# Kernel optimization log

Measured on AMD Instinct MI355X. Metric: run time of the kernel, lower is better.

Reference implementation:

```python
import jax, jax.numpy as jnp
import numpy as np

N, E, MUL, ATTR, NBASIS = 30000, 480000, 32, 8, 8
AVG_NEIGH = 16.0
INV_SQRT3 = 1.0 / np.sqrt(3.0).astype(np.float32)  # wigner 3j (1,1,0)
LOG2 = float(np.log(2.0))


def ssp(x):
    # shifted softplus: softplus(x) - log(2)
    return jax.nn.softplus(x) - LOG2


def setup_inputs() -> dict:
    key = jax.random.key(0)
    ks = jax.random.split(key, 15)
    return {
        "node_s": jax.random.normal(ks[0], (N, MUL), jnp.float32),
        "node_v": jax.random.normal(ks[1], (N, MUL, 3), jnp.float32),
        "node_attr": jax.random.uniform(ks[2], (N, ATTR), jnp.float32),
        "edge_attr": jax.random.normal(ks[3], (E, 4), jnp.float32),       # [sh0 | sh1(3)]
        "edge_scalars": jax.random.uniform(ks[4], (E, NBASIS), jnp.float32),
        "W1_0": jax.random.normal(ks[5], (MUL, MUL), jnp.float32),
        "W1_1": jax.random.normal(ks[6], (MUL, MUL), jnp.float32),
        "Wfc1": jax.random.normal(ks[7], (NBASIS, NBASIS), jnp.float32),
        "Wfc2": jax.random.normal(ks[8], (NBASIS, 4 * MUL), jnp.float32),
        "W2_0": jax.random.normal(ks[9], (2 * MUL, MUL), jnp.float32),
        "W2_1": jax.random.normal(ks[10], (2 * MUL, MUL), jnp.float32),
        "Wsc0": jax.random.normal(ks[11], (MUL, ATTR, MUL), jnp.float32),
        "Wsc1": jax.random.normal(ks[12], (MUL, ATTR, MUL), jnp.float32),
        "edge_src": jax.random.randint(ks[13], (E,), 0, N, jnp.int32),
        "edge_dst": jax.random.randint(ks[14], (E,), 0, N, jnp.int32),
    }


def reference(node_s, node_v, node_attr, edge_attr, edge_scalars,
              W1_0, W1_1, Wfc1, Wfc2, W2_0, W2_1, Wsc0, Wsc1,
              edge_src, edge_dst):
    n_nodes, mul = node_s.shape
    # --- fc: radial MLP -> per-edge TP weights (shared_weights=False) ---
    h = ssp(edge_scalars @ Wfc1 * (1.0 / np.sqrt(Wfc1.shape[0])))
    w = h @ Wfc2 * (1.0 / np.sqrt(Wfc2.shape[0]))                 # [E, 4*MUL]
    w00, w01, w10, w11 = jnp.split(w, 4, axis=1)                  # instruction order
    # --- lin1: per-irrep linear (fan-in normalized) ---
    inv_m = 1.0 / np.sqrt(mul)
    x0 = node_s @ W1_0 * inv_m                                    # [N, MUL]
    x1 = jnp.einsum('nud,uw->nwd', node_v, W1_1) * inv_m          # [N, MUL, 3]
    # --- gather destination-node features per edge ---
    x0d, x1d = x0[edge_dst], x1[edge_dst]
    sh0, sh1 = edge_attr[:, :1], edge_attr[:, 1:4]
    # --- uvu tensor product with per-edge weights ---
    s_a = w00 * x0d * sh0                                         # 0e x 0e -> 0e
    s_b = w11 * jnp.einsum('eud,ed->eu', x1d, sh1) * INV_SQRT3    # 1o x 1o -> 0e
    v_a = (w01 * x0d)[:, :, None] * sh1[:, None, :]               # 0e x 1o -> 1o
    v_b = w10[:, :, None] * x1d * sh0[:, :, None]                 # 1o x 0e -> 1o
    mid_s = jnp.concatenate([s_a, s_b], axis=1)                   # [E, 64]  (64x0e)
    mid_v = jnp.concatenate([v_a, v_b], axis=1)                   # [E, 64, 3] (64x1o)
    # --- scatter-sum over edge_src, normalized by sqrt(avg_num_neighbors) ---
    inv_nb = 1.0 / np.sqrt(AVG_NEIGH)
    agg_s = jax.ops.segment_sum(mid_s, edge_src, num_segments=n_nodes) * inv_nb
    agg_v = jax.ops.segment_sum(mid_v, edge_src, num_segments=n_nodes) * inv_nb
    # --- lin2 ---
    inv_2m = 1.0 / np.sqrt(2.0 * mul)
    out0 = agg_s @ W2_0 * inv_2m                                  # [N, MUL]
    out1 = jnp.einsum('nud,uw->nwd', agg_v, W2_1) * inv_2m        # [N, MUL, 3]
    # --- self-connection: fully-connected TP (attr is scalar 8x0e) ---
    sc_norm = 1.0 / np.sqrt(mul * node_attr.shape[1])
    sc0 = jnp.einsum('nu,nv,uvw->nw', node_s, node_attr, Wsc0) * sc_norm
    sc1 = jnp.einsum('nud,nv,uvw->nwd', node_v, node_attr, Wsc1) * sc_norm
    o0 = out0 + sc0
    o1 = out1 + sc1
    return jnp.concatenate([o0, o1.reshape(n_nodes, mul * 3)], axis=1)  # [N, 128]
```

## Files before the change

kernel.cpp:

```cpp
#include <hip/hip_runtime.h>
#include <math.h>

#define N_NODES 30000
#define N_EDGES 480000

typedef __attribute__((ext_vector_type(8))) short short8;
typedef __attribute__((ext_vector_type(4))) float f32x4;
typedef __attribute__((ext_vector_type(2))) float f32x2;

__device__ __forceinline__ unsigned short f2bf(float f) {
    unsigned u = __float_as_uint(f);
    u += 0x7fff + ((u >> 16) & 1);
    return (unsigned short)(u >> 16);
}
__device__ __forceinline__ float bfLO(unsigned v) { return __uint_as_float(v << 16); }
__device__ __forceinline__ float bfHI(unsigned v) { return __uint_as_float(v & 0xffff0000u); }
__device__ __forceinline__ unsigned packbf(float a, float b) {
    return (unsigned)f2bf(a) | ((unsigned)f2bf(b) << 16);
}
__device__ __forceinline__ unsigned ptk(float a, float b) {
    return (__float_as_uint(a) >> 16) | (__float_as_uint(b) & 0xffff0000u);
}

union U8 { short8 v; unsigned u[4]; };
union C4 { f32x4 v; float f[4]; };

#define VE(A, B, C, idx) ((idx) < 4 ? (&(A).x)[(idx)] : (idx) < 8 ? (&(B).x)[(idx) - 4] : (&(C).x)[(idx) - 8])

__global__ __launch_bounds__(256) void k_pre(
    const float* __restrict__ node_s,
    const float* __restrict__ node_v,
    const float* __restrict__ W1_0,
    const float* __restrict__ W1_1,
    const float* __restrict__ Wsc0,
    const float* __restrict__ Wsc1,
    const float* __restrict__ W2_0,
    const float* __restrict__ W2_1,
    const int* __restrict__ edge_src,
    int* __restrict__ deg,
    unsigned short* __restrict__ xnode,
    unsigned* __restrict__ bsc0,
    unsigned* __restrict__ bsc1,
    unsigned* __restrict__ b20,
    unsigned* __restrict__ b21)
{
    __shared__ unsigned sW1p[1024];
    int tid = threadIdx.x;

    if (blockIdx.x >= 1875) {
        int b = blockIdx.x - 1875;
        const float* Wm = (b == 0) ? Wsc0 : (b == 1) ? Wsc1 : (b == 2) ? W2_0 : W2_1;
        unsigned* dst = (b == 0) ? bsc0 : (b == 1) ? bsc1 : (b == 2) ? b20 : b21;
        float scale = (b < 2) ? 0.0625f : 0.03125f;
        int nu = (b < 2) ? 4096 : 1024;
        for (int idx = tid; idx < nu; idx += 256) {
            int jp = idx & 3;
            int lane = (idx >> 2) & 63;
            int ft = (idx >> 8) & 1;
            int kc = idx >> 9;
            int quad = lane >> 4, col = lane & 15;
            int k = kc * 32 + quad * 8 + jp * 2;
            int c = ft * 16 + col;
            dst[idx] = packbf(Wm[k * 32 + c] * scale, Wm[(k + 1) * 32 + c] * scale);
        }
        return;
    }

    atomicAdd(&deg[edge_src[blockIdx.x * 256 + tid]], 1);
    for (int i = tid; i < 1024; i += 256) sW1p[i] = packbf(W1_0[i], W1_1[i]);
    __syncthreads();

    int w = tid & 31;
    int n0 = blockIdx.x * 16 + (tid >> 5) * 2;
    const float inv_m = 0.1767766953f;
    float x0[2] = {0.f, 0.f}, x1a[2] = {0.f, 0.f};
    float x1b[2] = {0.f, 0.f}, x1c[2] = {0.f, 0.f};

    for (int uc = 0; uc < 32; uc += 4) {
        float4 sv[2], v0[2], v1[2], v2[2];
#pragma unroll
        for (int j = 0; j < 2; ++j) {
            sv[j] = *(const float4*)(node_s + (size_t)(n0 + j) * 32 + uc);
            const float* vp = node_v + (size_t)(n0 + j) * 96 + uc * 3;
            v0[j] = *(const float4*)(vp);
            v1[j] = *(const float4*)(vp + 4);
            v2[j] = *(const float4*)(vp + 8);
        }
#pragma unroll
        for (int kk = 0; kk < 4; ++kk) {
            int u = uc + kk;
            unsigned wp = sW1p[u * 32 + w];
            float w0k = bfLO(wp), w1k = bfHI(wp);
#pragma unroll
            for (int j = 0; j < 2; ++j) {
                float s  = (&sv[j].x)[kk];
                float vx = VE(v0[j], v1[j], v2[j], kk * 3 + 0);
                float vy = VE(v0[j], v1[j], v2[j], kk * 3 + 1);
                float vz = VE(v0[j], v1[j], v2[j], kk * 3 + 2);
                x0[j]  = fmaf(s,  w0k, x0[j]);
                x1a[j] = fmaf(vx, w1k, x1a[j]);
                x1b[j] = fmaf(vy, w1k, x1b[j]);
                x1c[j] = fmaf(vz, w1k, x1c[j]);
            }
        }
    }
#pragma unroll
    for (int j = 0; j < 2; ++j) {
        uint2 pk;
        pk.x = packbf(x0[j] * inv_m, x1a[j] * inv_m);
        pk.y = packbf(x1b[j] * inv_m, x1c[j] * inv_m);
        *(uint2*)(xnode + (size_t)(n0 + j) * 128 + w * 4) = pk;
    }
}

__global__ __launch_bounds__(1024) void scan_kernel(const int* __restrict__ deg,
                                                    int* __restrict__ offs,
                                                    int* __restrict__ cursor) {
    __shared__ int sdeg[N_NODES];
    __shared__ int wsum[16];
    int tid = threadIdx.x;
#pragma unroll
    for (int k = 0; k < 30; ++k) {
        int idx = k * 1024 + tid;
        if (idx < N_NODES) sdeg[idx] = deg[idx];
    }
    __syncthreads();
    int base = tid * 30;
    int s = 0;
    if (base < N_NODES) {
#pragma unroll
        for (int k = 0; k < 30; ++k) s += sdeg[base + k];
    }
    int lane = tid & 63, wid = tid >> 6;
    int inc = s;
#pragma unroll
    for (int d = 1; d < 64; d <<= 1) {
        int o = __shfl_up(inc, d, 64);
        if (lane >= d) inc += o;
    }
    if (lane == 63) wsum[wid] = inc;
    __syncthreads();
    if (tid < 16) {
        int v = wsum[tid];
        int t = v;
#pragma unroll
        for (int d = 1; d < 16; d <<= 1) {
            int o = __shfl_up(t, d, 64);
            if (tid >= d) t += o;
        }
        wsum[tid] = t - v;
    }
    __syncthreads();
    int run = inc - s + wsum[wid];
    if (base < N_NODES) {
#pragma unroll
        for (int k = 0; k < 30; ++k) {
            int n = base + k;
            int d = sdeg[n];
            sdeg[n] = run;
            run += d;
        }
    }
    __syncthreads();
#pragma unroll
    for (int k = 0; k < 30; ++k) {
        int idx = k * 1024 + tid;
        if (idx < N_NODES) {
            int v = sdeg[idx];
            offs[idx] = v;
            cursor[idx] = v;
        }
    }
    if (tid == 0) offs[N_NODES] = N_EDGES;
}

__global__ __launch_bounds__(256) void fill_kernel(
    const float* __restrict__ edge_attr,
    const float* __restrict__ edge_scalars,
    const float* __restrict__ Wfc1,
    const int* __restrict__ edge_src,
    const int* __restrict__ edge_dst,
    int* __restrict__ cursor,
    uint4* __restrict__ rec)
{
    __shared__ float sW[64];
    int tid = threadIdx.x;
    if (tid < 64) sW[tid] = Wfc1[tid];
    __syncthreads();

    int e = blockIdx.x * 256 + tid;
    float4 es0 = *(const float4*)(edge_scalars + (size_t)e * 8);
    float4 es1 = *(const float4*)(edge_scalars + (size_t)e * 8 + 4);
    float4 ea  = *(const float4*)(edge_attr + (size_t)e * 4);
    int src = edge_src[e];
    int dst = edge_dst[e];
    int pos = atomicAdd(&cursor[src], 1);

    const float inv8 = 0.3535533906f;
    float h[8];
#pragma unroll
    for (int i = 0; i < 8; ++i) {
        float acc = es0.x * sW[0 * 8 + i];
        acc = fmaf(es0.y, sW[1 * 8 + i], acc);
        acc = fmaf(es0.z, sW[2 * 8 + i], acc);
        acc = fmaf(es0.w, sW[3 * 8 + i], acc);
        acc = fmaf(es1.x, sW[4 * 8 + i], acc);
        acc = fmaf(es1.y, sW[5 * 8 + i], acc);
        acc = fmaf(es1.z, sW[6 * 8 + i], acc);
        acc = fmaf(es1.w, sW[7 * 8 + i], acc);
        acc *= inv8;
        float ax = fabsf(acc);
        float tt = __expf(-ax);
        h[i] = fmaxf(acc, 0.f) + __logf(1.f + tt) - 0.6931471806f;
    }
    uint4 r0, r1;
    r0.x = packbf(h[0], h[1]); r0.y = packbf(h[2], h[3]);
    r0.z = packbf(h[4], h[5]); r0.w = packbf(h[6], h[7]);
    r1.x = packbf(ea.x, ea.y); r1.y = packbf(ea.z, ea.w);
    r1.z = (unsigned)dst; r1.w = 0;
    rec[2 * pos]     = r0;
    rec[2 * pos + 1] = r1;
}

__global__ __launch_bounds__(256) void k_main(
    const int* __restrict__ offs,
    const uint4* __restrict__ rec,
    const float* __restrict__ Wfc2,
    const unsigned short* __restrict__ xnode,
    const float* __restrict__ node_s,
    const float* __restrict__ node_v,
    const float* __restrict__ node_attr,
    const unsigned* __restrict__ bsc0,
    const unsigned* __restrict__ bsc1,
    const unsigned* __restrict__ b20,
    const unsigned* __restrict__ b21,
    float* __restrict__ out)
{
    __shared__ float sS[16 * 33];
    __shared__ float sV[16 * 100];
    __shared__ unsigned short sAgg[16 * 264];
    int tid = threadIdx.x;
    int lane = tid & 63;
    int u = lane & 31;
    int half = lane >> 5;
    int wv = tid >> 6;
    int nbase = blockIdx.x * 16;

    for (int i = tid; i < 512; i += 256)
        sS[(i >> 5) * 33 + (i & 31)] = node_s[(size_t)nbase * 32 + i];
    for (int i = tid; i < 1536; i += 256)
        sV[(i / 96) * 100 + (i % 96)] = node_v[(size_t)nbase * 96 + i];

    const float inv8 = 0.3535533906f;
    const float inv_s3 = 0.5773502692f;
    f32x2 wfA[8], wfB[8];
#pragma unroll
    for (int i = 0; i < 8; ++i) {
        wfA[i].x = Wfc2[i * 128 + u] * inv8;
        wfA[i].y = Wfc2[i * 128 + 32 + u] * inv8;
        wfB[i].x = Wfc2[i * 128 + 64 + u] * inv8;
        wfB[i].y = Wfc2[i * 128 + 96 + u] * inv8 * inv_s3;
    }

    for (int jn = 0; jn < 4; ++jn) {
        int nl = wv * 4 + jn;
        int node = nbase + nl;
        int beg = offs[node], end = offs[node + 1];
        float a_sa = 0.f, a_sb = 0.f;
        float a_va0 = 0.f, a_va1 = 0.f, a_va2 = 0.f;
        float a_vb0 = 0.f, a_vb1 = 0.f, a_vb2 = 0.f;

        if (end > beg) {
            int last = end - 1;
            int i = beg + half;
            int p = min(i, last);
            uint4 a0 = rec[2 * p], a1 = rec[2 * p + 1];
            p = min(i + 2, last);
            uint4 b0 = rec[2 * p], b1 = rec[2 * p + 1];
            p = min(i + 4, last);
            uint4 c0 = rec[2 * p], c1 = rec[2 * p + 1];
            uint2 xA = *(const uint2*)(xnode + (size_t)(int)a1.z * 128 + u * 4);
            uint2 xB = *(const uint2*)(xnode + (size_t)(int)b1.z * 128 + u * 4);

            for (; i < end; i += 2) {
                int pD = min(i + 6, last);
                uint4 d0 = rec[2 * pD], d1 = rec[2 * pD + 1];
                uint2 xC = *(const uint2*)(xnode + (size_t)(int)c1.z * 128 + u * 4);

                float hv[8];
                hv[0] = bfLO(a0.x); hv[1] = bfHI(a0.x);
                hv[2] = bfLO(a0.y); hv[3] = bfHI(a0.y);
                hv[4] = bfLO(a0.z); hv[5] = bfHI(a0.z);
                hv[6] = bfLO(a0.w); hv[7] = bfHI(a0.w);
                f32x2 aA = {0.f, 0.f}, aB = {0.f, 0.f};
#pragma unroll
                for (int q = 0; q < 8; ++q) {
                    f32x2 hh = {hv[q], hv[q]};
                    aA = __builtin_elementwise_fma(hh, wfA[q], aA);
                    aB = __builtin_elementwise_fma(hh, wfB[q], aB);
                }
                float a00 = aA.x, a01 = aA.y, a10 = aB.x, a11 = aB.y;

                float sh0 = bfLO(a1.x), s1xe = bfHI(a1.x);
                float s1ye = bfLO(a1.y), s1ze = bfHI(a1.y);
                float x0 = bfLO(xA.x), xd0 = bfHI(xA.x);
                float xd1 = bfLO(xA.y), xd2 = bfHI(xA.y);

                float dot = xd0 * s1xe + xd1 * s1ye + xd2 * s1ze;
                a_sa = fmaf(a00 * sh0, x0, a_sa);
                a_sb = fmaf(a11, dot, a_sb);
                float w01x0 = a01 * x0;
                a_va0 = fmaf(w01x0, s1xe, a_va0);
                a_va1 = fmaf(w01x0, s1ye, a_va1);
                a_va2 = fmaf(w01x0, s1ze, a_va2);
                float t10 = a10 * sh0;
                a_vb0 = fmaf(t10, xd0, a_vb0);
                a_vb1 = fmaf(t10, xd1, a_vb1);
                a_vb2 = fmaf(t10, xd2, a_vb2);

                a0 = b0; a1 = b1; xA = xB;
                b0 = c0; b1 = c1; xB = xC;
                c0 = d0; c1 = d1;
            }
        }
        a_sa  += __shfl_xor(a_sa, 32, 64);
        a_sb  += __shfl_xor(a_sb, 32, 64);
        a_va0 += __shfl_xor(a_va0, 32, 64);
        a_va1 += __shfl_xor(a_va1, 32, 64);
        a_va2 += __shfl_xor(a_va2, 32, 64);
        a_vb0 += __shfl_xor(a_vb0, 32, 64);
        a_vb1 += __shfl_xor(a_vb1, 32, 64);
        a_vb2 += __shfl_xor(a_vb2, 32, 64);

        unsigned short* ap = sAgg + nl * 264;
        if (half == 0) {
            ap[u]       = f2bf(a_sa);
            ap[32 + u]  = f2bf(a_sb);
            ap[64 + u]  = f2bf(a_va0);
            ap[96 + u]  = f2bf(a_vb0);
        } else {
            ap[128 + u] = f2bf(a_va1);
            ap[160 + u] = f2bf(a_vb1);
            ap[192 + u] = f2bf(a_va2);
            ap[224 + u] = f2bf(a_vb2);
        }
    }
    __syncthreads();

    int col = lane & 15;
    int quad = lane >> 4;
    int m = col;
    bool is_s = (wv == 0);
    int sub = wv - 1;

    const short* Bs = (const short*)(is_s ? bsc0 : bsc1);
    const short* B2 = (const short*)(is_s ? b20 : b21);

    int aBase, fbase, fstep, n_a;
    if (is_s) {
        aBase = m * 264;
        fbase = m * 33;
        fstep = 1;
        n_a = nbase + m;
    } else {
        int r16 = 16 * sub + m;
        int nl = r16 / 3;
        int dd = r16 - nl * 3;
        aBase = nl * 264 + 64 + 64 * dd;
        fbase = nl * 100 + dd;
        fstep = 3;
        n_a = nbase + nl;
    }
    float4 A0 = *(const float4*)(node_attr + (size_t)n_a * 8);
    float4 A1 = *(const float4*)(node_attr + (size_t)n_a * 8 + 4);
    float aa0 = A0.x, aa1 = A0.y, aa2 = A0.z, aa3 = A0.w;
    float aa4 = A1.x, aa5 = A1.y, aa6 = A1.z, aa7 = A1.w;

    f32x4 acc0 = {0.f, 0.f, 0.f, 0.f};
    f32x4 acc1 = {0.f, 0.f, 0.f, 0.f};

#pragma unroll
    for (int kc = 0; kc < 2; ++kc) {
        short8 af = *(const short8*)((const short*)sAgg + aBase + kc * 32 + quad * 8);
        short8 bf0 = *(const short8*)(B2 + ((kc * 2 + 0) * 64 + lane) * 8);
        short8 bf1 = *(const short8*)(B2 + ((kc * 2 + 1) * 64 + lane) * 8);
        acc0 = __builtin_amdgcn_mfma_f32_16x16x32_bf16(af, bf0, acc0, 0, 0, 0);
        acc1 = __builtin_amdgcn_mfma_f32_16x16x32_bf16(af, bf1, acc1, 0, 0, 0);
    }
    const float* Sf = is_s ? sS : sV;
#pragma unroll
    for (int kc = 0; kc < 8; ++kc) {
        int uu = kc * 4 + quad;
        float f = Sf[fbase + uu * fstep];
        U8 af;
        af.u[0] = ptk(f * aa0, f * aa1);
        af.u[1] = ptk(f * aa2, f * aa3);
        af.u[2] = ptk(f * aa4, f * aa5);
        af.u[3] = ptk(f * aa6, f * aa7);
        short8 bf0 = *(const short8*)(Bs + ((kc * 2 + 0) * 64 + lane) * 8);
        short8 bf1 = *(const short8*)(Bs + ((kc * 2 + 1) * 64 + lane) * 8);
        acc0 = __builtin_amdgcn_mfma_f32_16x16x32_bf16(af.v, bf0, acc0, 0, 0, 0);
        acc1 = __builtin_amdgcn_mfma_f32_16x16x32_bf16(af.v, bf1, acc1, 0, 0, 0);
    }

    C4 c0, c1;
    c0.v = acc0; c1.v = acc1;
    if (is_s) {
#pragma unroll
        for (int r = 0; r < 4; ++r) {
            int n = nbase + (quad << 2) + r;
            out[(size_t)n * 128 + col]      = c0.f[r];
            out[(size_t)n * 128 + col + 16] = c1.f[r];
        }
    } else {
#pragma unroll
        for (int r = 0; r < 4; ++r) {
            int rl = 16 * sub + (quad << 2) + r;
            int nn = rl / 3;
            int dd = rl - nn * 3;
            int n = nbase + nn;
            out[(size_t)n * 128 + 32 + 3 * col + dd]        = c0.f[r];
            out[(size_t)n * 128 + 32 + 3 * (col + 16) + dd] = c1.f[r];
        }
    }
}

extern "C" void kernel_launch(void* const* d_in, const int* in_sizes, int n_in,
                              void* d_out, int out_size, void* d_ws, size_t ws_size,
                              hipStream_t stream) {
    const float* node_s       = (const float*)d_in[0];
    const float* node_v       = (const float*)d_in[1];
    const float* node_attr    = (const float*)d_in[2];
    const float* edge_attr    = (const float*)d_in[3];
    const float* edge_scalars = (const float*)d_in[4];
    const float* W1_0 = (const float*)d_in[5];
    const float* W1_1 = (const float*)d_in[6];
    const float* Wfc1 = (const float*)d_in[7];
    const float* Wfc2 = (const float*)d_in[8];
    const float* W2_0 = (const float*)d_in[9];
    const float* W2_1 = (const float*)d_in[10];
    const float* Wsc0 = (const float*)d_in[11];
    const float* Wsc1 = (const float*)d_in[12];
    const int* edge_src = (const int*)d_in[13];
    const int* edge_dst = (const int*)d_in[14];

    char* ws = (char*)d_ws;
    unsigned short* xnode = (unsigned short*)(ws);
    uint4* rec            = (uint4*)(ws + 7680000);
    int* deg    = (int*)(ws + 23040000);
    int* offs   = (int*)(ws + 23160000);
    int* cursor = (int*)(ws + 23280016);
    unsigned* bsc0 = (unsigned*)(ws + 23400064);
    unsigned* bsc1 = (unsigned*)(ws + 23416448);
    unsigned* b20  = (unsigned*)(ws + 23432832);
    unsigned* b21  = (unsigned*)(ws + 23436928);

    hipMemsetAsync(deg, 0, (size_t)N_NODES * sizeof(int), stream);
    k_pre<<<1879, 256, 0, stream>>>(node_s, node_v, W1_0, W1_1, Wsc0, Wsc1,
                                    W2_0, W2_1, edge_src, deg, xnode,
                                    bsc0, bsc1, b20, b21);
    scan_kernel<<<1, 1024, 0, stream>>>(deg, offs, cursor);
    fill_kernel<<<1875, 256, 0, stream>>>(edge_attr, edge_scalars, Wfc1,
                                          edge_src, edge_dst, cursor, rec);
    k_main<<<1875, 256, 0, stream>>>(offs, rec, Wfc2, xnode,
                                     node_s, node_v, node_attr,
                                     bsc0, bsc1, b20, b21, (float*)d_out);
}
```

Baseline: 236.7 us.

## Compute lin1 node projections with bf16 MFMA and pack edge accumulators into f32x2 FMAs

The per-node lin1 linear (node_s@W1_0 and node_v einsum with W1_1) in k_pre is now done with 16x16x32 bf16 MFMA instructions. Vector inputs are transposed through shared memory and results are staged in LDS before packing to bf16. Separately, the edge aggregation loop packs pairs of vector accumulators into f32x2 elementwise FMAs to encourage packed-FMA issue. The MFMA path rounds inputs to bf16 before the multiply, which loses some precision, and it adds extra LDS traffic and barriers.

```diff
diff --git a/kernel.cpp b/kernel.cpp
--- a/kernel.cpp
+++ b/kernel.cpp
@@ -24,8 +24,6 @@
 
 union U8 { short8 v; unsigned u[4]; };
 union C4 { f32x4 v; float f[4]; };
-
-#define VE(A, B, C, idx) ((idx) < 4 ? (&(A).x)[(idx)] : (idx) < 8 ? (&(B).x)[(idx) - 4] : (&(C).x)[(idx) - 8])
 
 __global__ __launch_bounds__(256) void k_pre(
     const float* __restrict__ node_s,
@@ -44,7 +42,8 @@
     unsigned* __restrict__ b20,
     unsigned* __restrict__ b21)
 {
-    __shared__ unsigned sW1p[1024];
+    __shared__ float sVT[16 * 100];
+    __shared__ float sXo[16 * 140];
     int tid = threadIdx.x;
 
     if (blockIdx.x >= 1875) {
@@ -67,49 +66,76 @@
     }
 
     atomicAdd(&deg[edge_src[blockIdx.x * 256 + tid]], 1);
-    for (int i = tid; i < 1024; i += 256) sW1p[i] = packbf(W1_0[i], W1_1[i]);
-    __syncthreads();
-
-    int w = tid & 31;
-    int n0 = blockIdx.x * 16 + (tid >> 5) * 2;
+
+    int nbase = blockIdx.x * 16;
+    for (int i = tid; i < 1536; i += 256) {
+        int nl = i / 96, r = i - nl * 96;
+        int u = r / 3, d = r - u * 3;
+        sVT[nl * 100 + d * 32 + u] = node_v[(size_t)nbase * 96 + i];
+    }
+    __syncthreads();
+
+    int lane = tid & 63;
+    int wv = tid >> 6;
+    int col = lane & 15, quad = lane >> 4, m = lane & 15;
+
+    const float* W1 = (wv == 0) ? W1_0 : W1_1;
+    U8 bf0, bf1;
+#pragma unroll
+    for (int p = 0; p < 4; ++p) {
+        int k = quad * 8 + 2 * p;
+        bf0.u[p] = packbf(W1[k * 32 + col],      W1[(k + 1) * 32 + col]);
+        bf1.u[p] = packbf(W1[k * 32 + col + 16], W1[(k + 1) * 32 + col + 16]);
+    }
+
+    U8 af;
+    if (wv == 0) {
+        const float* sp = node_s + (size_t)(nbase + m) * 32 + quad * 8;
+        float4 a0 = *(const float4*)(sp);
+        float4 a1 = *(const float4*)(sp + 4);
+        af.u[0] = packbf(a0.x, a0.y); af.u[1] = packbf(a0.z, a0.w);
+        af.u[2] = packbf(a1.x, a1.y); af.u[3] = packbf(a1.z, a1.w);
+    } else {
+        int R = 16 * (wv - 1) + m;
+        int nl = R / 3, d = R - nl * 3;
+        const float* vp = sVT + nl * 100 + d * 32 + quad * 8;
+        af.u[0] = packbf(vp[0], vp[1]); af.u[1] = packbf(vp[2], vp[3]);
+        af.u[2] = packbf(vp[4], vp[5]); af.u[3] = packbf(vp[6], vp[7]);
+    }
+
+    f32x4 acc0 = {0.f, 0.f, 0.f, 0.f};
+    f32x4 acc1 = {0.f, 0.f, 0.f, 0.f};
+    acc0 = __builtin_amdgcn_mfma_f32_16x16x32_bf16(af.v, bf0.v, acc0, 0, 0, 0);
+    acc1 = __builtin_amdgcn_mfma_f32_16x16x32_bf16(af.v, bf1.v, acc1, 0, 0, 0);
+
+    C4 c0, c1;
+    c0.v = acc0; c1.v = acc1;
+    if (wv == 0) {
+#pragma unroll
+        for (int r = 0; r < 4; ++r) {
+            int nl = (quad << 2) + r;
+            sXo[nl * 140 + col]      = c0.f[r];
+            sXo[nl * 140 + col + 16] = c1.f[r];
+        }
+    } else {
+#pragma unroll
+        for (int r = 0; r < 4; ++r) {
+            int R = 16 * (wv - 1) + (quad << 2) + r;
+            int nl = R / 3, d = R - nl * 3;
+            sXo[nl * 140 + (1 + d) * 34 + col]      = c0.f[r];
+            sXo[nl * 140 + (1 + d) * 34 + col + 16] = c1.f[r];
+        }
+    }
+    __syncthreads();
+
     const float inv_m = 0.1767766953f;
-    float x0[2] = {0.f, 0.f}, x1a[2] = {0.f, 0.f};
-    float x1b[2] = {0.f, 0.f}, x1c[2] = {0.f, 0.f};
-
-    for (int uc = 0; uc < 32; uc += 4) {
-        float4 sv[2], v0[2], v1[2], v2[2];
-#pragma unroll
-        for (int j = 0; j < 2; ++j) {
-            sv[j] = *(const float4*)(node_s + (size_t)(n0 + j) * 32 + uc);
-            const float* vp = node_v + (size_t)(n0 + j) * 96 + uc * 3;
-            v0[j] = *(const float4*)(vp);
-            v1[j] = *(const float4*)(vp + 4);
-            v2[j] = *(const float4*)(vp + 8);
-        }
-#pragma unroll
-        for (int kk = 0; kk < 4; ++kk) {
-            int u = uc + kk;
-            unsigned wp = sW1p[u * 32 + w];
-            float w0k = bfLO(wp), w1k = bfHI(wp);
-#pragma unroll
-            for (int j = 0; j < 2; ++j) {
-                float s  = (&sv[j].x)[kk];
-                float vx = VE(v0[j], v1[j], v2[j], kk * 3 + 0);
-                float vy = VE(v0[j], v1[j], v2[j], kk * 3 + 1);
-                float vz = VE(v0[j], v1[j], v2[j], kk * 3 + 2);
-                x0[j]  = fmaf(s,  w0k, x0[j]);
-                x1a[j] = fmaf(vx, w1k, x1a[j]);
-                x1b[j] = fmaf(vy, w1k, x1b[j]);
-                x1c[j] = fmaf(vz, w1k, x1c[j]);
-            }
-        }
-    }
-#pragma unroll
-    for (int j = 0; j < 2; ++j) {
+    for (int i = tid; i < 512; i += 256) {
+        int nl = i >> 5, u = i & 31;
+        const float* xp = sXo + nl * 140;
         uint2 pk;
-        pk.x = packbf(x0[j] * inv_m, x1a[j] * inv_m);
-        pk.y = packbf(x1b[j] * inv_m, x1c[j] * inv_m);
-        *(uint2*)(xnode + (size_t)(n0 + j) * 128 + w * 4) = pk;
+        pk.x = packbf(xp[u] * inv_m,       xp[34 + u] * inv_m);
+        pk.y = packbf(xp[68 + u] * inv_m,  xp[102 + u] * inv_m);
+        *(uint2*)(xnode + (size_t)(nbase + nl) * 128 + u * 4) = pk;
     }
 }
 
@@ -267,8 +293,8 @@
         int node = nbase + nl;
         int beg = offs[node], end = offs[node + 1];
         float a_sa = 0.f, a_sb = 0.f;
-        float a_va0 = 0.f, a_va1 = 0.f, a_va2 = 0.f;
-        float a_vb0 = 0.f, a_vb1 = 0.f, a_vb2 = 0.f;
+        f32x2 a_va01 = {0.f, 0.f}, a_vb01 = {0.f, 0.f};
+        float a_va2 = 0.f, a_vb2 = 0.f;
 
         if (end > beg) {
             int last = end - 1;
@@ -310,12 +336,14 @@
                 a_sa = fmaf(a00 * sh0, x0, a_sa);
                 a_sb = fmaf(a11, dot, a_sb);
                 float w01x0 = a01 * x0;
-                a_va0 = fmaf(w01x0, s1xe, a_va0);
-                a_va1 = fmaf(w01x0, s1ye, a_va1);
+                float t10 = a10 * sh0;
+                f32x2 wb = {w01x0, w01x0};
+                f32x2 tb = {t10, t10};
+                f32x2 s01 = {s1xe, s1ye};
+                f32x2 xd01 = {xd0, xd1};
+                a_va01 = __builtin_elementwise_fma(wb, s01, a_va01);
+                a_vb01 = __builtin_elementwise_fma(tb, xd01, a_vb01);
                 a_va2 = fmaf(w01x0, s1ze, a_va2);
-                float t10 = a10 * sh0;
-                a_vb0 = fmaf(t10, xd0, a_vb0);
-                a_vb1 = fmaf(t10, xd1, a_vb1);
                 a_vb2 = fmaf(t10, xd2, a_vb2);
 
                 a0 = b0; a1 = b1; xA = xB;
@@ -323,24 +351,24 @@
                 c0 = d0; c1 = d1;
             }
         }
-        a_sa  += __shfl_xor(a_sa, 32, 64);
-        a_sb  += __shfl_xor(a_sb, 32, 64);
-        a_va0 += __shfl_xor(a_va0, 32, 64);
-        a_va1 += __shfl_xor(a_va1, 32, 64);
-        a_va2 += __shfl_xor(a_va2, 32, 64);
-        a_vb0 += __shfl_xor(a_vb0, 32, 64);
-        a_vb1 += __shfl_xor(a_vb1, 32, 64);
-        a_vb2 += __shfl_xor(a_vb2, 32, 64);
+        a_sa    += __shfl_xor(a_sa, 32, 64);
+        a_sb    += __shfl_xor(a_sb, 32, 64);
+        a_va01.x += __shfl_xor(a_va01.x, 32, 64);
+        a_va01.y += __shfl_xor(a_va01.y, 32, 64);
+        a_vb01.x += __shfl_xor(a_vb01.x, 32, 64);
+        a_vb01.y += __shfl_xor(a_vb01.y, 32, 64);
+        a_va2   += __shfl_xor(a_va2, 32, 64);
+        a_vb2   += __shfl_xor(a_vb2, 32, 64);
 
         unsigned short* ap = sAgg + nl * 264;
         if (half == 0) {
             ap[u]       = f2bf(a_sa);
             ap[32 + u]  = f2bf(a_sb);
-            ap[64 + u]  = f2bf(a_va0);
-            ap[96 + u]  = f2bf(a_vb0);
+            ap[64 + u]  = f2bf(a_va01.x);
+            ap[96 + u]  = f2bf(a_vb01.x);
         } else {
-            ap[128 + u] = f2bf(a_va1);
-            ap[160 + u] = f2bf(a_vb1);
+            ap[128 + u] = f2bf(a_va01.y);
+            ap[160 + u] = f2bf(a_vb01.y);
             ap[192 + u] = f2bf(a_va2);
             ap[224 + u] = f2bf(a_vb2);
         }
```

New measurement: 229.5 us. 3.0% less time.
